# Performance work log

Measured on AMD Instinct MI355X. Metric: run time of the kernel, lower is better.

Reference implementation:

```python
import jax, jax.numpy as jnp
from jax import lax
import numpy as np
import math

EPS = 1e-6

def _np(a, s=1.0):
    return np.asarray(a, dtype=np.float32) * np.float32(s)

def _gabor(theta, sigma=1.1, lambd=3.0, gamma=0.65):
    c = np.arange(-2, 3, dtype=np.float32)
    yy, xx = np.meshgrid(c, c, indexing='ij')
    xt = xx * math.cos(theta) + yy * math.sin(theta)
    yt = -xx * math.sin(theta) + yy * math.cos(theta)
    k = np.exp(-(xt**2 + gamma**2 * yt**2) / (2.0 * sigma**2)) * np.cos(2.0 * math.pi * xt / lambd)
    k = k - k.mean()
    return (k / max(np.abs(k).sum(), 1e-6)).astype(np.float32)

def _dct_like(u=2, v=2, size=5):
    c = np.arange(size, dtype=np.float32)
    yy, xx = np.meshgrid(c, c, indexing='ij')
    k = np.cos(math.pi*(2*xx+1)*u/(2*size)) * np.cos(math.pi*(2*yy+1)*v/(2*size))
    k = k - k.mean()
    return (k / max(np.abs(k).sum(), 1e-6)).astype(np.float32)

# stacked 3x3 stencils: laplacian, hess_xx, hess_yy, hess_xy, sobel_x, sobel_y, diag_main, diag_anti, checkerboard
_K3 = np.stack([
    _np([[0,1,0],[1,-4,1],[0,1,0]]),
    _np([[0,0,0],[1,-2,1],[0,0,0]]),
    _np([[0,1,0],[0,-2,0],[0,1,0]]),
    _np([[1,0,-1],[0,0,0],[-1,0,1]], 0.25),
    _np([[-1,0,1],[-2,0,2],[-1,0,1]], 0.125),
    _np([[-1,-2,-1],[0,0,0],[1,2,1]], 0.125),
    _np([[-2,-1,0],[-1,0,1],[0,1,2]], 0.125),
    _np([[0,1,2],[-1,0,1],[-2,-1,0]], 0.125),
    _np([[1,-1,1],[-1,1,-1],[1,-1,1]], 1.0/9.0),
])[:, None]

_Z5 = np.zeros((5,5), np.float32)

def _row5(vals):
    k = _Z5.copy(); k[2, :] = vals; return k

def _col5(vals):
    k = _Z5.copy(); k[:, 2] = vals; return k

# stacked 5x5 stencils: ha_second_h, ha_second_v, ha_green_h, ha_green_v, mhc_green, stripe_x, stripe_y, gabor45, gabor135, dct
_K5 = np.stack([
    _row5([-0.5, 0.0, 1.0, 0.0, -0.5]),
    _col5([-0.5, 0.0, 1.0, 0.0, -0.5]),
    _row5([-0.25, 0.5, 0.5, 0.5, -0.25]),
    _col5([-0.25, 0.5, 0.5, 0.5, -0.25]),
    _np([[0,0,-1,0,0],[0,0,2,0,0],[-1,2,4,2,-1],[0,0,2,0,0],[0,0,-1,0,0]], 0.125),
    _row5([0.25, -1.0, 1.5, -1.0, 0.25]),
    _col5([0.25, -1.0, 1.5, -1.0, 0.25]),
    _gabor(math.pi/4.0),
    _gabor(3.0*math.pi/4.0),
    _dct_like(),
])[:, None]

_SMOOTH5 = (_np([[1,2,3,2,1],[2,4,6,4,2],[3,6,9,6,3],[2,4,6,4,2],[1,2,3,2,1]]) / np.float32(81.0))[None, None]

K3 = jnp.asarray(_K3)
K5 = jnp.asarray(_K5)
SMOOTH5 = jnp.asarray(_SMOOTH5)

def _masks(H, W):
    # gbrg pattern
    z = lambda: np.zeros((1, 1, H, W), np.float32)
    r, b, gr, gb, row, col = z(), z(), z(), z(), z(), z()
    row[:, :, 1::2, :] = 1.0
    col[:, :, :, 1::2] = 1.0
    gb[:, :, 0::2, 0::2] = 1.0
    b[:, :, 0::2, 1::2] = 1.0
    r[:, :, 1::2, 0::2] = 1.0
    gr[:, :, 1::2, 1::2] = 1.0
    g = gr + gb
    return tuple(jnp.asarray(a) for a in (r, g, b, gr, gb, row, col))

def _pad(x, ph, pw):
    return jnp.pad(x, ((0, 0), (0, 0), (ph, ph), (pw, pw)), mode='reflect')

def _conv_same(x, k, groups=1):
    kh, kw = k.shape[-2:]
    return lax.conv_general_dilated(_pad(x, kh // 2, kw // 2), k.astype(x.dtype), (1, 1), 'VALID',
                                    dimension_numbers=('NCHW', 'OIHW', 'NCHW'),
                                    feature_group_count=groups)

def _avg_same(x, kh, kw):
    k = jnp.full((1, 1, kh, kw), 1.0 / (kh * kw), x.dtype)
    return _conv_same(x, k)

def _forward(bayer):
    B, _, H, W = bayer.shape
    r, g, b, gr, gb, row, col = _masks(H, W)
    c3 = _conv_same(bayer, K3)  # [B,9,H,W]
    lap, hxx, hyy, hxy, gx, gy, gdm, gda, chk = jnp.split(c3, 9, axis=1)
    c5 = _conv_same(bayer, K5)  # [B,10,H,W]
    hsh, hsv, hgh, hgv, mhcf, stx, sty, g45, g135, dctp = jnp.split(c5, 10, axis=1)
    # morphological gradient: 3x3 max - min (reflect-padded)
    xp = _pad(bayer, 1, 1)
    mgrad = (lax.reduce_window(xp, -jnp.inf, lax.max, (1, 1, 3, 3), (1, 1, 1, 1), 'VALID')
             - lax.reduce_window(xp, jnp.inf, lax.min, (1, 1, 3, 3), (1, 1, 1, 1), 'VALID'))
    gmag = jnp.sqrt(gx * gx + gy * gy + EPS)
    # structure tensor (3x3 box smoothing of gradient outer products)
    jxx = _avg_same(gx * gx, 3, 3)
    jyy = _avg_same(gy * gy, 3, 3)
    jxy = _avg_same(gx * gy, 3, 3)
    tr = jxx + jyy
    lam_gap = jnp.sqrt((jxx - jyy) ** 2 + 4.0 * jxy * jxy + EPS)
    coherence = lam_gap / (tr + EPS)
    anisotropy = (jxx - jyy) / (tr + EPS)
    ha_dis = jnp.abs(hgh - hgv)
    res_h = bayer - hgh
    res_v = bayer - hgv
    res_eh = _avg_same(res_h * res_h, 3, 3)
    res_ev = _avg_same(res_v * res_v, 3, 3)
    dgd = jnp.abs(gx) - jnp.abs(gy)
    dsd = jnp.abs(hxx) - jnp.abs(hyy)
    # 1x5 / 5x1 line variances
    mh = _avg_same(bayer, 1, 5)
    mv = _avg_same(bayer, 5, 1)
    lvh = jnp.maximum(_avg_same(bayer * bayer, 1, 5) - mh * mh, 0.0)
    lvv = jnp.maximum(_avg_same(bayer * bayer, 5, 1) - mv * mv, 0.0)
    lvd = lvh - lvv
    dconf = jnp.abs(lvd) / (lvh + lvv + EPS)
    # normalized sparse fills (smooth5 of masked signal / smooth5 of mask)
    mstack = jnp.concatenate([r, g, b, gr, gb], axis=1)  # [1,5,H,W]
    sig = bayer * mstack  # [B,5,H,W]
    ks = jnp.tile(SMOOTH5, (5, 1, 1, 1))
    num = _conv_same(sig, ks, groups=5)
    den = jnp.maximum(_conv_same(mstack, ks, groups=5), EPS)
    rf, gf, bf, grf, gbf = jnp.split(num / den, 5, axis=1)
    rg = rf - gf
    bg = bf - gf
    gpd = grf - gbf
    mhc = jnp.where(g > 0.5, bayer, mhcf)
    mhc_ha = mhc - 0.5 * (hgh + hgv)
    rres = (bayer - mhc) * r
    bres = (bayer - mhc) * b
    chk_e = _avg_same(chk * chk, 3, 3)
    str_e = _avg_same(stx * stx + sty * sty, 3, 3)
    lmean = _avg_same(bayer, 3, 3)
    lvar = jnp.maximum(_avg_same(bayer * bayer, 3, 3) - lmean * lmean, 0.0)
    gen = _avg_same(gx * gx + gy * gy, 3, 3)
    bm = lambda m: jnp.broadcast_to(m, bayer.shape)
    feats = [bm(r), bm(g), bm(b), bm(gr), bm(gb), bm(row), bm(col),
             lap, hxx, hyy, hxy, mgrad, gx, gy, gdm, gda, gmag,
             coherence, anisotropy, hsh, hsv, hgh, hgv, ha_dis,
             res_h, res_v, res_eh, res_ev, dgd, dsd, lvh, lvv, lvd, dconf,
             rg, bg, gpd, mhc, mhc_ha, rres, bres,
             stx, sty, chk, g45, g135, dctp, chk_e, str_e, lmean, lvar, gen]
    return jnp.concatenate(feats, axis=1)  # [B,52,H,W]

def setup_inputs() -> dict:
    key = jax.random.key(0)
    bayer = jax.random.uniform(key, (2, 1, 768, 768), dtype=jnp.float32)
    return {"bayer": bayer}

def reference(bayer):
    return _forward(bayer)
```

## Files before the change

kernel.cpp:

```cpp
#include <hip/hip_runtime.h>
#include <math.h>

#define H_ 768
#define W_ 768
#define TY 16
#define TX 64
#define NTHREADS 256
#define EPS_ 1e-6f

typedef float f4 __attribute__((ext_vector_type(4)));

__device__ __forceinline__ f4 mk4(float x, float y, float z, float w){ f4 r; r.x=x; r.y=y; r.z=z; r.w=w; return r; }
__device__ __forceinline__ f4 sp(float s){ return mk4(s,s,s,s); }
__device__ __forceinline__ f4 max4(f4 a, f4 b){ return mk4(fmaxf(a.x,b.x),fmaxf(a.y,b.y),fmaxf(a.z,b.z),fmaxf(a.w,b.w)); }
__device__ __forceinline__ f4 min4(f4 a, f4 b){ return mk4(fminf(a.x,b.x),fminf(a.y,b.y),fminf(a.z,b.z),fminf(a.w,b.w)); }
__device__ __forceinline__ f4 sqrt4(f4 a){ return mk4(sqrtf(a.x),sqrtf(a.y),sqrtf(a.z),sqrtf(a.w)); }
__device__ __forceinline__ f4 abs4(f4 a){ return mk4(fabsf(a.x),fabsf(a.y),fabsf(a.z),fabsf(a.w)); }
__device__ __forceinline__ float rcp1(float x){
#if __has_builtin(__builtin_amdgcn_rcpf)
    return __builtin_amdgcn_rcpf(x);
#else
    return 1.0f / x;
#endif
}
__device__ __forceinline__ f4 rcp4(f4 a){ return mk4(rcp1(a.x),rcp1(a.y),rcp1(a.z),rcp1(a.w)); }

__device__ __forceinline__ int refl(int c, int n) {
    c = c < 0 ? -c : c;
    return c >= n ? 2 * n - 2 - c : c;
}

__global__ __launch_bounds__(NTHREADS)
void bayer_feat(const float* __restrict__ in, float* __restrict__ out) {
    const int bz  = blockIdx.z;
    const int gy0 = blockIdx.y * TY;
    const int gx0 = blockIdx.x * TX;
    const int tid = threadIdx.x;
    const float* src = in + (size_t)bz * (H_ * W_);

    __shared__ float sB[TY + 6][TX + 7];
    __shared__ float sE[7][TY + 2][TX + 3];

    for (int i = tid; i < (TY + 6) * (TX + 6); i += NTHREADS) {
        int r = i / (TX + 6), c = i - r * (TX + 6);
        sB[r][c] = src[refl(gy0 - 3 + r, H_) * W_ + refl(gx0 - 3 + c, W_)];
    }
    __syncthreads();

    for (int i = tid; i < (TY + 2) * (TX + 2); i += NTHREADS) {
        int ey = i / (TX + 2), ex = i - ey * (TX + 2);
        int sy = refl(gy0 - 1 + ey, H_) - gy0 + 3;
        int sx = refl(gx0 - 1 + ex, W_) - gx0 + 3;
        float a00 = sB[sy-1][sx-1], a01 = sB[sy-1][sx], a02 = sB[sy-1][sx+1];
        float a10 = sB[sy  ][sx-1], a11 = sB[sy  ][sx], a12 = sB[sy  ][sx+1];
        float a20 = sB[sy+1][sx-1], a21 = sB[sy+1][sx], a22 = sB[sy+1][sx+1];
        float l2 = sB[sy][sx-2], r2 = sB[sy][sx+2];
        float u2 = sB[sy-2][sx], d2 = sB[sy+2][sx];
        sE[0][ey][ex] = 0.125f * (-a00 + a02 - 2.f*a10 + 2.f*a12 - a20 + a22);
        sE[1][ey][ex] = 0.125f * (-a00 - 2.f*a01 - a02 + a20 + 2.f*a21 + a22);
        sE[2][ey][ex] = -0.25f*(l2 + r2) + 0.5f*(a10 + a11 + a12);
        sE[3][ey][ex] = -0.25f*(u2 + d2) + 0.5f*(a01 + a11 + a21);
        sE[4][ey][ex] = (a00 - a01 + a02 - a10 + a11 - a12 + a20 - a21 + a22) * (1.f/9.f);
        sE[5][ey][ex] = 0.25f*(l2 + r2) - (a10 + a12) + 1.5f*a11;
        sE[6][ey][ex] = 0.25f*(u2 + d2) - (a01 + a21) + 1.5f*a11;
    }
    __syncthreads();

    const int lq  = tid & 15;
    const int ly  = tid >> 4;
    const int lx4 = lq * 4;
    const int gy  = gy0 + ly, gx = gx0 + lx4;
    const int py  = gy & 1;
    const int syc = ly + 3;
    const int ey  = ly + 1;
    const int exb = lx4 + 1;
    const size_t HW = (size_t)H_ * W_;
    float* po = out + (size_t)bz * 52 * HW + (size_t)gy * W_ + gx;

#define ST(c, v) __builtin_nontemporal_store((v), (f4*)(po + (size_t)(c) * HW))

    float a[5][8];
#pragma unroll
    for (int r = 0; r < 5; ++r)
#pragma unroll
        for (int i = 0; i < 8; ++i)
            a[r][i] = sB[syc - 2 + r][lx4 + 1 + i];

#define AV(r, i) mk4(a[r][i], a[r][(i)+1], a[r][(i)+2], a[r][(i)+3])
#define SL(arr, o) mk4(arr[o], arr[(o)+1], arr[(o)+2], arr[(o)+3])

    const f4 zero4 = sp(0.f);
    const f4 ev01  = mk4(0,1,0,1);
    const f4 ev10  = mk4(1,0,1,0);
    const float inv9 = 1.f / 9.f;

    ST(0, py ? ev10 : zero4);
    ST(1, py ? ev01 : ev10);
    ST(2, py ? zero4 : ev01);
    ST(3, py ? ev01 : zero4);
    ST(4, py ? zero4 : ev10);
    ST(5, sp((float)py));
    ST(6, ev01);

    f4 jxx = zero4, jyy = zero4, jxy = zero4, reh = zero4, rev = zero4, cke = zero4, ste = zero4;
    f4 gxv = zero4, gyv = zero4, hghv = zero4, hgvv = zero4, chkv = zero4, stxv = zero4, styv = zero4;
#pragma unroll
    for (int dy = -1; dy <= 1; ++dy) {
        float g_[6], h_[6], hh_[6], hv_[6], ck_[6], sx_[6], sy_[6];
#pragma unroll
        for (int j = 0; j < 6; ++j) {
            g_[j]  = sE[0][ey+dy][exb-1+j];
            h_[j]  = sE[1][ey+dy][exb-1+j];
            hh_[j] = sE[2][ey+dy][exb-1+j];
            hv_[j] = sE[3][ey+dy][exb-1+j];
            ck_[j] = sE[4][ey+dy][exb-1+j];
            sx_[j] = sE[5][ey+dy][exb-1+j];
            sy_[j] = sE[6][ey+dy][exb-1+j];
        }
        f4 bm_ = AV(dy+2, 1), b0_ = AV(dy+2, 2), bp_ = AV(dy+2, 3);
#pragma unroll
        for (int o = 0; o < 3; ++o) {
            f4 q = SL(g_, o), w = SL(h_, o);
            jxx += q*q; jyy += w*w; jxy += q*w;
            if (dy == 0 && o == 1) { gxv = q; gyv = w; }
            f4 bb = (o == 0) ? bm_ : (o == 1 ? b0_ : bp_);
            f4 rh = bb - SL(hh_, o); reh += rh*rh;
            f4 rv = bb - SL(hv_, o); rev += rv*rv;
            if (dy == 0 && o == 1) { hghv = SL(hh_, 1); hgvv = SL(hv_, 1); }
            f4 cc = SL(ck_, o); cke += cc*cc;
            if (dy == 0 && o == 1) chkv = cc;
            f4 s1 = SL(sx_, o), s2 = SL(sy_, o);
            ste += s1*s1 + s2*s2;
            if (dy == 0 && o == 1) { stxv = s1; styv = s2; }
        }
    }
    jxx = jxx * sp(inv9); jyy = jyy * sp(inv9); jxy = jxy * sp(inv9);

    f4 ctr = AV(2,2);
    ST(12, gxv); ST(13, gyv);
    ST(16, sqrt4(gxv*gxv + gyv*gyv + sp(EPS_)));
    f4 trc = jxx + jyy;
    f4 dj  = jxx - jyy;
    f4 lam = sqrt4(dj*dj + sp(4.f)*jxy*jxy + sp(EPS_));
    f4 itr = rcp4(trc + sp(EPS_));
    ST(17, lam * itr);
    ST(18, dj * itr);
    ST(21, hghv); ST(22, hgvv);
    ST(23, abs4(hghv - hgvv));
    ST(24, ctr - hghv); ST(25, ctr - hgvv);
    ST(26, reh * sp(inv9)); ST(27, rev * sp(inv9));
    ST(28, abs4(gxv) - abs4(gyv));
    ST(41, stxv); ST(42, styv); ST(43, chkv);
    ST(47, cke * sp(inv9)); ST(48, ste * sp(inv9));
    ST(51, trc);

    f4 lap = AV(1,2) + AV(2,1) - sp(4.f)*ctr + AV(2,3) + AV(3,2);
    f4 hxx = AV(2,1) - sp(2.f)*ctr + AV(2,3);
    f4 hyy = AV(1,2) - sp(2.f)*ctr + AV(3,2);
    f4 hxy = sp(0.25f)*(AV(1,1) - AV(1,3) - AV(3,1) + AV(3,3));
    ST(7, lap); ST(8, hxx); ST(9, hyy); ST(10, hxy);
    ST(29, abs4(hxx) - abs4(hyy));

    {
        f4 mx = AV(1,1), mn = mx;
#pragma unroll
        for (int r = 1; r <= 3; ++r)
#pragma unroll
            for (int i = 1; i <= 3; ++i) { f4 v = AV(r,i); mx = max4(mx, v); mn = min4(mn, v); }
        ST(11, mx - mn);
    }

    ST(14, sp(0.125f)*(sp(-2.f)*AV(1,1) - AV(1,2) - AV(2,1) + AV(2,3) + AV(3,2) + sp(2.f)*AV(3,3)));
    ST(15, sp(0.125f)*(AV(1,2) + sp(2.f)*AV(1,3) - AV(2,1) + AV(2,3) - sp(2.f)*AV(3,1) - AV(3,2)));
    ST(19, sp(-0.5f)*(AV(2,0) + AV(2,4)) + ctr);
    ST(20, sp(-0.5f)*(AV(0,2) + AV(4,2)) + ctr);

    {
        f4 sh = AV(2,0)+AV(2,1)+AV(2,2)+AV(2,3)+AV(2,4);
        f4 qh = AV(2,0)*AV(2,0)+AV(2,1)*AV(2,1)+AV(2,2)*AV(2,2)+AV(2,3)*AV(2,3)+AV(2,4)*AV(2,4);
        f4 sv_ = AV(0,2)+AV(1,2)+AV(2,2)+AV(3,2)+AV(4,2);
        f4 qv_ = AV(0,2)*AV(0,2)+AV(1,2)*AV(1,2)+AV(2,2)*AV(2,2)+AV(3,2)*AV(3,2)+AV(4,2)*AV(4,2);
        f4 mh = sh * sp(0.2f), mv = sv_ * sp(0.2f);
        f4 lvh = max4(qh*sp(0.2f) - mh*mh, zero4);
        f4 lvv = max4(qv_*sp(0.2f) - mv*mv, zero4);
        ST(30, lvh); ST(31, lvv);
        f4 lvd = lvh - lvv;
        ST(32, lvd);
        ST(33, abs4(lvd) * rcp4(lvh + lvv + sp(EPS_)));
    }

    {
        f4 t0 = zero4, t1 = zero4, t2 = zero4, t3 = zero4;
#pragma unroll
        for (int r = 0; r < 5; ++r) {
            f4 E = AV(r,0) + sp(3.f)*AV(r,2) + AV(r,4);
            f4 O = sp(2.f)*(AV(r,1) + AV(r,3));
            f4 rE = mk4(E.x, O.y, E.z, O.w);
            f4 rO = mk4(O.x, E.y, O.z, E.w);
            if (r == 0 || r == 4)      { t0 += rE;          t2 += rO; }
            else if (r == 2)           { t0 += sp(3.f)*rE;  t2 += sp(3.f)*rO; }
            else                       { t1 += sp(2.f)*rE;  t3 += sp(2.f)*rO; }
        }
        f4 cEE = py ? t1 : t0, cOE = py ? t0 : t1, cEO = py ? t3 : t2, cOO = py ? t2 : t3;
        const f4 inv_r  = py ? mk4(0.04f,0.05f,0.04f,0.05f)     : mk4(0.05f,0.0625f,0.05f,0.0625f);
        const f4 inv_b  = py ? mk4(0.0625f,0.05f,0.0625f,0.05f) : mk4(0.05f,0.04f,0.05f,0.04f);
        const f4 inv_gr = py ? mk4(0.05f,0.04f,0.05f,0.04f)     : mk4(0.0625f,0.05f,0.0625f,0.05f);
        const f4 inv_gb = py ? mk4(0.05f,0.0625f,0.05f,0.0625f) : mk4(0.04f,0.05f,0.04f,0.05f);
        const f4 inv_g  = py ? mk4(1.f/40.f,1.f/41.f,1.f/40.f,1.f/41.f)
                             : mk4(1.f/41.f,1.f/40.f,1.f/41.f,1.f/40.f);
        f4 rfv = cOE*inv_r, bfv = cEO*inv_b, grfv = cOO*inv_gr, gbfv = cEE*inv_gb;
        f4 gfv = (cEE + cOO)*inv_g;
        ST(34, rfv - gfv); ST(35, bfv - gfv); ST(36, grfv - gbfv);
    }

    {
        f4 mhcf = sp(0.125f)*( -AV(0,2) + sp(2.f)*AV(1,2) - AV(2,0) + sp(2.f)*AV(2,1) + sp(4.f)*ctr
                               + sp(2.f)*AV(2,3) - AV(2,4) + sp(2.f)*AV(3,2) - AV(4,2) );
        f4 mhc = py ? mk4(mhcf.x, ctr.y, mhcf.z, ctr.w) : mk4(ctr.x, mhcf.y, ctr.z, mhcf.w);
        ST(37, mhc);
        ST(38, mhc - sp(0.5f)*(hghv + hgvv));
        f4 dif = ctr - mhc;
        ST(39, dif * (py ? ev10 : zero4));
        ST(40, dif * (py ? zero4 : ev01));
    }

    {
        const float G45[5][5] = {
            {-0.002092f, -0.015195f, -0.063321f, -0.002285f,  0.036511f},
            {-0.015195f, -0.086304f,  0.003803f,  0.119456f, -0.002285f},
            {-0.063321f,  0.003803f,  0.172851f,  0.003803f, -0.063321f},
            {-0.002285f,  0.119456f,  0.003803f, -0.086304f, -0.015195f},
            { 0.036511f, -0.002285f, -0.063321f, -0.015195f, -0.002092f}
        };
        const float ADC[5] = {0.25f, -0.09549150f, -0.30901699f, -0.09549150f, 0.25f};
        f4 s45 = zero4, s135 = zero4, dct = zero4;
#pragma unroll
        for (int r = 0; r < 5; ++r) {
            f4 t = zero4;
#pragma unroll
            for (int i = 0; i < 5; ++i) {
                f4 v = AV(r, i);
                s45  += sp(G45[r][i])     * v;
                s135 += sp(G45[r][4 - i]) * v;
                t    += sp(ADC[i])        * v;
            }
            dct += sp(ADC[r]) * t;
        }
        ST(44, s45); ST(45, s135); ST(46, dct);
    }

    {
        f4 s3 = zero4, q3 = zero4;
#pragma unroll
        for (int r = 1; r <= 3; ++r)
#pragma unroll
            for (int i = 1; i <= 3; ++i) { f4 v = AV(r,i); s3 += v; q3 += v*v; }
        f4 lmean = s3 * sp(inv9);
        ST(49, lmean);
        ST(50, max4(q3*sp(inv9) - lmean*lmean, zero4));
    }

#undef ST
#undef AV
#undef SL
}

extern "C" void kernel_launch(void* const* d_in, const int* in_sizes, int n_in,
                              void* d_out, int out_size, void* d_ws, size_t ws_size,
                              hipStream_t stream) {
    (void)n_in; (void)d_ws; (void)ws_size; (void)out_size;
    const float* bayer = (const float*)d_in[0];
    float* out = (float*)d_out;
    const int B = in_sizes[0] / (H_ * W_);
    dim3 grid(W_ / TX, H_ / TY, B);
    bayer_feat<<<grid, NTHREADS, 0, stream>>>(bayer, out);
}
```

Baseline: 56.21 us.

## Reorder feature computation to cut register pressure and use plain stores

Sets a minimum of four blocks per multiprocessor in launch bounds and reorders the per-pixel feature computations so each group's live values are freed sooner. Center values of the edge-filter maps are reloaded from shared memory rather than kept live across the loop, and the 3x3 max/min and mean/variance passes are merged into one loop. The nontemporal output stores become ordinary vector stores. Lower register use could raise occupancy, but the launch-bound cap may cause spills, and dropping nontemporal stores changes how the large 52-channel output passes through the cache.

```diff
diff --git a/kernel.cpp b/kernel.cpp
--- a/kernel.cpp
+++ b/kernel.cpp
@@ -30,7 +30,7 @@
     return c >= n ? 2 * n - 2 - c : c;
 }
 
-__global__ __launch_bounds__(NTHREADS)
+__global__ __launch_bounds__(NTHREADS, 4)
 void bayer_feat(const float* __restrict__ in, float* __restrict__ out) {
     const int bz  = blockIdx.z;
     const int gy0 = blockIdx.y * TY;
@@ -69,124 +69,55 @@
     const int lq  = tid & 15;
     const int ly  = tid >> 4;
     const int lx4 = lq * 4;
-    const int gy  = gy0 + ly, gx = gx0 + lx4;
+    const int gy  = gy0 + ly;
     const int py  = gy & 1;
     const int syc = ly + 3;
     const int ey  = ly + 1;
     const int exb = lx4 + 1;
     const size_t HW = (size_t)H_ * W_;
-    float* po = out + (size_t)bz * 52 * HW + (size_t)gy * W_ + gx;
-
-#define ST(c, v) __builtin_nontemporal_store((v), (f4*)(po + (size_t)(c) * HW))
-
-    float a[5][8];
-#pragma unroll
-    for (int r = 0; r < 5; ++r)
-#pragma unroll
-        for (int i = 0; i < 8; ++i)
-            a[r][i] = sB[syc - 2 + r][lx4 + 1 + i];
-
+    float* po = out + (size_t)bz * 52 * HW + (size_t)gy * W_ + (gx0 + lx4);
+
+#define ST(c, v) *(f4*)(po + (size_t)(c) * HW) = (v)
 #define AV(r, i) mk4(a[r][i], a[r][(i)+1], a[r][(i)+2], a[r][(i)+3])
 #define SL(arr, o) mk4(arr[o], arr[(o)+1], arr[(o)+2], arr[(o)+3])
+#define CTR(f) mk4(sE[f][ey][exb], sE[f][ey][exb+1], sE[f][ey][exb+2], sE[f][ey][exb+3])
 
     const f4 zero4 = sp(0.f);
     const f4 ev01  = mk4(0,1,0,1);
     const f4 ev10  = mk4(1,0,1,0);
     const float inv9 = 1.f / 9.f;
 
-    ST(0, py ? ev10 : zero4);
-    ST(1, py ? ev01 : ev10);
-    ST(2, py ? zero4 : ev01);
-    ST(3, py ? ev01 : zero4);
-    ST(4, py ? zero4 : ev10);
-    ST(5, sp((float)py));
-    ST(6, ev01);
-
-    f4 jxx = zero4, jyy = zero4, jxy = zero4, reh = zero4, rev = zero4, cke = zero4, ste = zero4;
-    f4 gxv = zero4, gyv = zero4, hghv = zero4, hgvv = zero4, chkv = zero4, stxv = zero4, styv = zero4;
-#pragma unroll
-    for (int dy = -1; dy <= 1; ++dy) {
-        float g_[6], h_[6], hh_[6], hv_[6], ck_[6], sx_[6], sy_[6];
-#pragma unroll
-        for (int j = 0; j < 6; ++j) {
-            g_[j]  = sE[0][ey+dy][exb-1+j];
-            h_[j]  = sE[1][ey+dy][exb-1+j];
-            hh_[j] = sE[2][ey+dy][exb-1+j];
-            hv_[j] = sE[3][ey+dy][exb-1+j];
-            ck_[j] = sE[4][ey+dy][exb-1+j];
-            sx_[j] = sE[5][ey+dy][exb-1+j];
-            sy_[j] = sE[6][ey+dy][exb-1+j];
+    float a[5][8];
+#pragma unroll
+    for (int r = 0; r < 5; ++r)
+#pragma unroll
+        for (int i = 0; i < 8; ++i)
+            a[r][i] = sB[syc - 2 + r][lx4 + 1 + i];
+
+
+    {
+        const float G45[5][5] = {
+            {-0.002092f, -0.015195f, -0.063321f, -0.002285f,  0.036511f},
+            {-0.015195f, -0.086304f,  0.003803f,  0.119456f, -0.002285f},
+            {-0.063321f,  0.003803f,  0.172851f,  0.003803f, -0.063321f},
+            {-0.002285f,  0.119456f,  0.003803f, -0.086304f, -0.015195f},
+            { 0.036511f, -0.002285f, -0.063321f, -0.015195f, -0.002092f}
+        };
+        const float ADC[5] = {0.25f, -0.09549150f, -0.30901699f, -0.09549150f, 0.25f};
+        f4 s45 = zero4, s135 = zero4, dct = zero4;
+#pragma unroll
+        for (int r = 0; r < 5; ++r) {
+            f4 t = zero4;
+#pragma unroll
+            for (int i = 0; i < 5; ++i) {
+                f4 v = AV(r, i);
+                s45  += sp(G45[r][i])     * v;
+                s135 += sp(G45[r][4 - i]) * v;
+                t    += sp(ADC[i])        * v;
+            }
+            dct += sp(ADC[r]) * t;
         }
-        f4 bm_ = AV(dy+2, 1), b0_ = AV(dy+2, 2), bp_ = AV(dy+2, 3);
-#pragma unroll
-        for (int o = 0; o < 3; ++o) {
-            f4 q = SL(g_, o), w = SL(h_, o);
-            jxx += q*q; jyy += w*w; jxy += q*w;
-            if (dy == 0 && o == 1) { gxv = q; gyv = w; }
-            f4 bb = (o == 0) ? bm_ : (o == 1 ? b0_ : bp_);
-            f4 rh = bb - SL(hh_, o); reh += rh*rh;
-            f4 rv = bb - SL(hv_, o); rev += rv*rv;
-            if (dy == 0 && o == 1) { hghv = SL(hh_, 1); hgvv = SL(hv_, 1); }
-            f4 cc = SL(ck_, o); cke += cc*cc;
-            if (dy == 0 && o == 1) chkv = cc;
-            f4 s1 = SL(sx_, o), s2 = SL(sy_, o);
-            ste += s1*s1 + s2*s2;
-            if (dy == 0 && o == 1) { stxv = s1; styv = s2; }
-        }
-    }
-    jxx = jxx * sp(inv9); jyy = jyy * sp(inv9); jxy = jxy * sp(inv9);
-
-    f4 ctr = AV(2,2);
-    ST(12, gxv); ST(13, gyv);
-    ST(16, sqrt4(gxv*gxv + gyv*gyv + sp(EPS_)));
-    f4 trc = jxx + jyy;
-    f4 dj  = jxx - jyy;
-    f4 lam = sqrt4(dj*dj + sp(4.f)*jxy*jxy + sp(EPS_));
-    f4 itr = rcp4(trc + sp(EPS_));
-    ST(17, lam * itr);
-    ST(18, dj * itr);
-    ST(21, hghv); ST(22, hgvv);
-    ST(23, abs4(hghv - hgvv));
-    ST(24, ctr - hghv); ST(25, ctr - hgvv);
-    ST(26, reh * sp(inv9)); ST(27, rev * sp(inv9));
-    ST(28, abs4(gxv) - abs4(gyv));
-    ST(41, stxv); ST(42, styv); ST(43, chkv);
-    ST(47, cke * sp(inv9)); ST(48, ste * sp(inv9));
-    ST(51, trc);
-
-    f4 lap = AV(1,2) + AV(2,1) - sp(4.f)*ctr + AV(2,3) + AV(3,2);
-    f4 hxx = AV(2,1) - sp(2.f)*ctr + AV(2,3);
-    f4 hyy = AV(1,2) - sp(2.f)*ctr + AV(3,2);
-    f4 hxy = sp(0.25f)*(AV(1,1) - AV(1,3) - AV(3,1) + AV(3,3));
-    ST(7, lap); ST(8, hxx); ST(9, hyy); ST(10, hxy);
-    ST(29, abs4(hxx) - abs4(hyy));
-
-    {
-        f4 mx = AV(1,1), mn = mx;
-#pragma unroll
-        for (int r = 1; r <= 3; ++r)
-#pragma unroll
-            for (int i = 1; i <= 3; ++i) { f4 v = AV(r,i); mx = max4(mx, v); mn = min4(mn, v); }
-        ST(11, mx - mn);
-    }
-
-    ST(14, sp(0.125f)*(sp(-2.f)*AV(1,1) - AV(1,2) - AV(2,1) + AV(2,3) + AV(3,2) + sp(2.f)*AV(3,3)));
-    ST(15, sp(0.125f)*(AV(1,2) + sp(2.f)*AV(1,3) - AV(2,1) + AV(2,3) - sp(2.f)*AV(3,1) - AV(3,2)));
-    ST(19, sp(-0.5f)*(AV(2,0) + AV(2,4)) + ctr);
-    ST(20, sp(-0.5f)*(AV(0,2) + AV(4,2)) + ctr);
-
-    {
-        f4 sh = AV(2,0)+AV(2,1)+AV(2,2)+AV(2,3)+AV(2,4);
-        f4 qh = AV(2,0)*AV(2,0)+AV(2,1)*AV(2,1)+AV(2,2)*AV(2,2)+AV(2,3)*AV(2,3)+AV(2,4)*AV(2,4);
-        f4 sv_ = AV(0,2)+AV(1,2)+AV(2,2)+AV(3,2)+AV(4,2);
-        f4 qv_ = AV(0,2)*AV(0,2)+AV(1,2)*AV(1,2)+AV(2,2)*AV(2,2)+AV(3,2)*AV(3,2)+AV(4,2)*AV(4,2);
-        f4 mh = sh * sp(0.2f), mv = sv_ * sp(0.2f);
-        f4 lvh = max4(qh*sp(0.2f) - mh*mh, zero4);
-        f4 lvv = max4(qv_*sp(0.2f) - mv*mv, zero4);
-        ST(30, lvh); ST(31, lvv);
-        f4 lvd = lvh - lvv;
-        ST(32, lvd);
-        ST(33, abs4(lvd) * rcp4(lvh + lvv + sp(EPS_)));
+        ST(44, s45); ST(45, s135); ST(46, dct);
     }
 
     {
@@ -213,6 +144,26 @@
         ST(34, rfv - gfv); ST(35, bfv - gfv); ST(36, grfv - gbfv);
     }
 
+    f4 ctr = AV(2,2);
+
+    {
+        f4 sh = AV(2,0)+AV(2,1)+ctr+AV(2,3)+AV(2,4);
+        f4 qh = AV(2,0)*AV(2,0)+AV(2,1)*AV(2,1)+ctr*ctr+AV(2,3)*AV(2,3)+AV(2,4)*AV(2,4);
+        f4 sv_ = AV(0,2)+AV(1,2)+ctr+AV(3,2)+AV(4,2);
+        f4 qv_ = AV(0,2)*AV(0,2)+AV(1,2)*AV(1,2)+ctr*ctr+AV(3,2)*AV(3,2)+AV(4,2)*AV(4,2);
+        f4 mh = sh * sp(0.2f), mv = sv_ * sp(0.2f);
+        f4 lvh = max4(qh*sp(0.2f) - mh*mh, zero4);
+        f4 lvv = max4(qv_*sp(0.2f) - mv*mv, zero4);
+        ST(30, lvh); ST(31, lvv);
+        f4 lvd = lvh - lvv;
+        ST(32, lvd);
+        ST(33, abs4(lvd) * rcp4(lvh + lvv + sp(EPS_)));
+    }
+
+    ST(19, sp(-0.5f)*(AV(2,0) + AV(2,4)) + ctr);
+    ST(20, sp(-0.5f)*(AV(0,2) + AV(4,2)) + ctr);
+
+    f4 hghv = CTR(2), hgvv = CTR(3);
     {
         f4 mhcf = sp(0.125f)*( -AV(0,2) + sp(2.f)*AV(1,2) - AV(2,0) + sp(2.f)*AV(2,1) + sp(4.f)*ctr
                                + sp(2.f)*AV(2,3) - AV(2,4) + sp(2.f)*AV(3,2) - AV(4,2) );
@@ -223,46 +174,97 @@
         ST(39, dif * (py ? ev10 : zero4));
         ST(40, dif * (py ? zero4 : ev01));
     }
-
-    {
-        const float G45[5][5] = {
-            {-0.002092f, -0.015195f, -0.063321f, -0.002285f,  0.036511f},
-            {-0.015195f, -0.086304f,  0.003803f,  0.119456f, -0.002285f},
-            {-0.063321f,  0.003803f,  0.172851f,  0.003803f, -0.063321f},
-            {-0.002285f,  0.119456f,  0.003803f, -0.086304f, -0.015195f},
-            { 0.036511f, -0.002285f, -0.063321f, -0.015195f, -0.002092f}
-        };
-        const float ADC[5] = {0.25f, -0.09549150f, -0.30901699f, -0.09549150f, 0.25f};
-        f4 s45 = zero4, s135 = zero4, dct = zero4;
-#pragma unroll
-        for (int r = 0; r < 5; ++r) {
-            f4 t = zero4;
-#pragma unroll
-            for (int i = 0; i < 5; ++i) {
-                f4 v = AV(r, i);
-                s45  += sp(G45[r][i])     * v;
-                s135 += sp(G45[r][4 - i]) * v;
-                t    += sp(ADC[i])        * v;
-            }
-            dct += sp(ADC[r]) * t;
-        }
-        ST(44, s45); ST(45, s135); ST(46, dct);
-    }
-
-    {
-        f4 s3 = zero4, q3 = zero4;
+    ST(21, hghv); ST(22, hgvv);
+    ST(23, abs4(hghv - hgvv));
+    ST(24, ctr - hghv); ST(25, ctr - hgvv);
+
+    {
+        f4 lap = AV(1,2) + AV(2,1) - sp(4.f)*ctr + AV(2,3) + AV(3,2);
+        f4 hxx = AV(2,1) - sp(2.f)*ctr + AV(2,3);
+        f4 hyy = AV(1,2) - sp(2.f)*ctr + AV(3,2);
+        f4 hxy = sp(0.25f)*(AV(1,1) - AV(1,3) - AV(3,1) + AV(3,3));
+        ST(7, lap); ST(8, hxx); ST(9, hyy); ST(10, hxy);
+        ST(29, abs4(hxx) - abs4(hyy));
+    }
+    ST(14, sp(0.125f)*(sp(-2.f)*AV(1,1) - AV(1,2) - AV(2,1) + AV(2,3) + AV(3,2) + sp(2.f)*AV(3,3)));
+    ST(15, sp(0.125f)*(AV(1,2) + sp(2.f)*AV(1,3) - AV(2,1) + AV(2,3) - sp(2.f)*AV(3,1) - AV(3,2)));
+
+    {
+        f4 mx = AV(1,1), mn = mx, s3 = zero4, q3 = zero4;
 #pragma unroll
         for (int r = 1; r <= 3; ++r)
 #pragma unroll
-            for (int i = 1; i <= 3; ++i) { f4 v = AV(r,i); s3 += v; q3 += v*v; }
+            for (int i = 1; i <= 3; ++i) {
+                f4 v = AV(r,i);
+                mx = max4(mx, v); mn = min4(mn, v);
+                s3 += v; q3 += v*v;
+            }
+        ST(11, mx - mn);
         f4 lmean = s3 * sp(inv9);
         ST(49, lmean);
         ST(50, max4(q3*sp(inv9) - lmean*lmean, zero4));
     }
 
+    {
+        f4 gxv = CTR(0), gyv = CTR(1);
+        ST(12, gxv); ST(13, gyv);
+        ST(16, sqrt4(gxv*gxv + gyv*gyv + sp(EPS_)));
+        ST(28, abs4(gxv) - abs4(gyv));
+    }
+    ST(41, CTR(5)); ST(42, CTR(6)); ST(43, CTR(4));
+
+    {
+        f4 jxx = zero4, jyy = zero4, jxy = zero4, reh = zero4, rev = zero4, cke = zero4, ste = zero4;
+#pragma unroll
+        for (int dy = -1; dy <= 1; ++dy) {
+            float g_[6], h_[6], hh_[6], hv_[6], ck_[6], sx_[6], sy_[6];
+#pragma unroll
+            for (int j = 0; j < 6; ++j) {
+                g_[j]  = sE[0][ey+dy][exb-1+j];
+                h_[j]  = sE[1][ey+dy][exb-1+j];
+                hh_[j] = sE[2][ey+dy][exb-1+j];
+                hv_[j] = sE[3][ey+dy][exb-1+j];
+                ck_[j] = sE[4][ey+dy][exb-1+j];
+                sx_[j] = sE[5][ey+dy][exb-1+j];
+                sy_[j] = sE[6][ey+dy][exb-1+j];
+            }
+            f4 bm_ = AV(dy+2, 1), b0_ = AV(dy+2, 2), bp_ = AV(dy+2, 3);
+#pragma unroll
+            for (int o = 0; o < 3; ++o) {
+                f4 q = SL(g_, o), w = SL(h_, o);
+                jxx += q*q; jyy += w*w; jxy += q*w;
+                f4 bb = (o == 0) ? bm_ : (o == 1 ? b0_ : bp_);
+                f4 rh = bb - SL(hh_, o); reh += rh*rh;
+                f4 rv = bb - SL(hv_, o); rev += rv*rv;
+                f4 cc = SL(ck_, o); cke += cc*cc;
+                f4 s1 = SL(sx_, o), s2 = SL(sy_, o);
+                ste += s1*s1 + s2*s2;
+            }
+        }
+        jxx = jxx * sp(inv9); jyy = jyy * sp(inv9); jxy = jxy * sp(inv9);
+        f4 trc = jxx + jyy;
+        f4 dj  = jxx - jyy;
+        f4 lam = sqrt4(dj*dj + sp(4.f)*jxy*jxy + sp(EPS_));
+        f4 itr = rcp4(trc + sp(EPS_));
+        ST(17, lam * itr);
+        ST(18, dj * itr);
+        ST(51, trc);
+        ST(26, reh * sp(inv9)); ST(27, rev * sp(inv9));
+        ST(47, cke * sp(inv9)); ST(48, ste * sp(inv9));
+    }
+
+    ST(0, py ? ev10 : zero4);
+    ST(1, py ? ev01 : ev10);
+    ST(2, py ? zero4 : ev01);
+    ST(3, py ? ev01 : zero4);
+    ST(4, py ? zero4 : ev10);
+    ST(5, sp((float)py));
+    ST(6, ev01);
+
 #undef ST
 #undef AV
 #undef SL
+#undef CTR
 }
 
 extern "C" void kernel_launch(void* const* d_in, const int* in_sizes, int n_in,
```

Result: faster. 46.09 us (-18.0%).
